# Kernel optimization log

Measured on AMD Instinct MI355X. Metric: run time of the kernel, lower is better.

## Reference

```python
import jax, jax.numpy as jnp
import numpy as np

N_NODES = 25000
N_EDGES = 400000
N_GRAPHS = 1000
HID = 185
IN_CH = 9
EPS = 1e-5  # BatchNorm eps (eval mode: uses running stats)


def setup_inputs() -> dict:
    key = jax.random.key(0)
    ks = jax.random.split(key, 12)
    x = jax.random.normal(ks[0], (N_NODES, IN_CH), jnp.float32)
    edge_index = jax.random.randint(ks[1], (2, N_EDGES), 0, N_NODES, jnp.int32)
    batch = jnp.sort(jax.random.randint(ks[2], (N_NODES,), 0, N_GRAPHS, jnp.int32))
    W0 = jax.random.normal(ks[3], (IN_CH, HID), jnp.float32) * 0.3
    b0 = jnp.zeros((HID,), jnp.float32)
    W_h = jax.random.normal(ks[4], (3, HID, HID), jnp.float32) * 0.07
    b_h = jnp.zeros((3, HID), jnp.float32)
    bn_gamma = 1.0 + 0.1 * jax.random.normal(ks[5], (4, HID), jnp.float32)
    bn_beta = 0.1 * jax.random.normal(ks[6], (4, HID), jnp.float32)
    bn_mean = 0.1 * jax.random.normal(ks[7], (4, HID), jnp.float32)
    bn_var = jax.random.uniform(ks[8], (4, HID), jnp.float32, 0.5, 1.5)
    W_jk = jax.random.normal(ks[9], (4 * HID, HID), jnp.float32) * 0.05
    b_jk = jnp.zeros((HID,), jnp.float32)
    W_out = jax.random.normal(ks[10], (HID, 1), jnp.float32) * 0.1
    b_out = jnp.zeros((1,), jnp.float32)
    return dict(x=x, edge_index=edge_index, batch=batch, W0=W0, b0=b0,
                W_h=W_h, b_h=b_h, bn_gamma=bn_gamma, bn_beta=bn_beta,
                bn_mean=bn_mean, bn_var=bn_var, W_jk=W_jk, b_jk=b_jk,
                W_out=W_out, b_out=b_out)


def reference(x, edge_index, batch, W0, b0, W_h, b_h, bn_gamma, bn_beta,
              bn_mean, bn_var, W_jk, b_jk, W_out, b_out):
    N = x.shape[0]
    # GCN normalization with self-loops (gcn_norm, edge_weight = 1)
    loop = jnp.arange(N, dtype=edge_index.dtype)
    src = jnp.concatenate([edge_index[0], loop])  # [E+N]
    dst = jnp.concatenate([edge_index[1], loop])  # [E+N]
    deg = jax.ops.segment_sum(jnp.ones_like(dst, dtype=x.dtype), dst, num_segments=N)
    dis = jnp.where(deg > 0, jax.lax.rsqrt(jnp.maximum(deg, 1.0)), 0.0)
    enorm = dis[src] * dis[dst]  # [E+N]

    def gcn_conv(h, W, b):
        h = h @ W                                   # [N, HID]
        msg = h[src] * enorm[:, None]               # gather + scale, [E+N, HID]
        return jax.ops.segment_sum(msg, dst, num_segments=N) + b

    def bn_relu(h, i):
        h = (h - bn_mean[i]) * jax.lax.rsqrt(bn_var[i] + EPS) * bn_gamma[i] + bn_beta[i]
        return jax.nn.relu(h)  # dropout is identity in eval mode

    xs = []
    h = bn_relu(gcn_conv(x, W0, b0), 0)
    xs.append(h)
    for i in range(3):
        h = bn_relu(gcn_conv(h, W_h[i], b_h[i]), i + 1)
        xs.append(h)
    # JumpingKnowledge 'cat' + internal lin (740 -> 185)
    h = jnp.concatenate(xs, axis=-1) @ W_jk + b_jk  # [N, HID]
    # global_max_pool over graphs
    pooled = jax.ops.segment_max(h, batch, num_segments=N_GRAPHS)  # [G, HID]
    return pooled @ W_out + b_out  # [G, 1]
```

## Files before the change

### kernel.cpp

```cpp
#include <hip/hip_runtime.h>
#include <hip/hip_bf16.h>

#define N_NODES 25000
#define N_EDGES 400000
#define N_GRAPHS 1000
#define HID 185
#define EPS 1e-5f
#define XPITCH 768
#define APITCH 36

typedef __attribute__((ext_vector_type(8))) short bf16x8;
typedef __attribute__((ext_vector_type(4))) float f32x4;

__device__ __forceinline__ short f2bf(float f) {
    union { float f; unsigned u; } v; v.f = f;
    unsigned r = v.u + 0x7FFFu + ((v.u >> 16) & 1u);
    return (short)(r >> 16);
}
__device__ __forceinline__ float bfl(unsigned u) { return __uint_as_float(u << 16); }
__device__ __forceinline__ float bfh(unsigned u) { return __uint_as_float(u & 0xFFFF0000u); }
__device__ __forceinline__ unsigned pk2(float lo, float hi) {
    return (unsigned)(unsigned short)f2bf(lo) | ((unsigned)(unsigned short)f2bf(hi) << 16);
}

__global__ void k_init(int* cnt, int* cursor) {
    int i = blockIdx.x * blockDim.x + threadIdx.x;
    if (i < N_NODES) { cnt[i] = 0; cursor[i] = 0; }
}

__global__ void k_deg(const int* __restrict__ dst, int* cnt, int E) {
    int i = blockIdx.x * blockDim.x + threadIdx.x;
    if (i < E) atomicAdd(&cnt[dst[i]], 1);
}

__global__ void k_dis(const int* __restrict__ cnt, float* dis, int N) {
    int i = blockIdx.x * blockDim.x + threadIdx.x;
    if (i < N) dis[i] = rsqrtf((float)(cnt[i] + 1));
}

__global__ __launch_bounds__(256) void k_scan_part(const int* __restrict__ cnt,
                                                   int* __restrict__ bsum, int N) {
    int i = blockIdx.x * 256 + threadIdx.x;
    int v = (i < N) ? cnt[i] : 0;
    #pragma unroll
    for (int off = 32; off; off >>= 1) v += __shfl_down(v, off);
    __shared__ int s[4];
    if ((threadIdx.x & 63) == 0) s[threadIdx.x >> 6] = v;
    __syncthreads();
    if (threadIdx.x == 0) bsum[blockIdx.x] = s[0] + s[1] + s[2] + s[3];
}

__global__ __launch_bounds__(128) void k_scan_mid(const int* __restrict__ bsum,
                                                  int* __restrict__ boff, int NB) {
    __shared__ int s[128];
    int t = threadIdx.x;
    int v = (t < NB) ? bsum[t] : 0;
    s[t] = v; __syncthreads();
    for (int off = 1; off < 128; off <<= 1) {
        int x = (t >= off) ? s[t - off] : 0;
        __syncthreads();
        s[t] += x;
        __syncthreads();
    }
    if (t < NB) boff[t] = s[t] - v;
}

__global__ __launch_bounds__(256) void k_scan_add(const int* __restrict__ cnt,
                                                  const int* __restrict__ boff,
                                                  int* __restrict__ rowptr, int N) {
    __shared__ int s[256];
    int t = threadIdx.x;
    int i = blockIdx.x * 256 + t;
    int v = (i < N) ? cnt[i] : 0;
    s[t] = v; __syncthreads();
    for (int off = 1; off < 256; off <<= 1) {
        int x = (t >= off) ? s[t - off] : 0;
        __syncthreads();
        s[t] += x;
        __syncthreads();
    }
    if (i < N) rowptr[i + 1] = boff[blockIdx.x] + s[t];
    if (i == 0) rowptr[0] = 0;
}

__global__ void k_scatter(const int* __restrict__ src, const int* __restrict__ dst,
                          const float* __restrict__ dis, const int* __restrict__ rowptr,
                          int* cursor, int* __restrict__ csr_src,
                          float* __restrict__ csr_w, int E) {
    int e = blockIdx.x * blockDim.x + threadIdx.x;
    if (e < E) {
        int d = dst[e];
        int s = src[e];
        int pos = atomicAdd(&cursor[d], 1);
        int o = rowptr[d] + pos;
        csr_src[o] = s;
        csr_w[o] = dis[s];
    }
}

__global__ void k_prep_w(const float* __restrict__ W_h, const float* __restrict__ W_jk,
                         const float* __restrict__ b0, const float* __restrict__ b_h,
                         const float* __restrict__ gamma, const float* __restrict__ beta,
                         const float* __restrict__ mean, const float* __restrict__ var,
                         short* __restrict__ Wt_h, short* __restrict__ Wt_jk,
                         float* __restrict__ bnsc, float* __restrict__ bnsh) {
    int idx = blockIdx.x * 256 + threadIdx.x;
    const int HW = 3 * 192 * 192;
    const int JW = 192 * 768;
    if (idx < HW) {
        int l = idx / (192 * 192);
        int r = idx % (192 * 192);
        int n = r / 192, k = r % 192;
        float v = (n < HID && k < HID) ? W_h[(l * HID + k) * HID + n] : 0.0f;
        Wt_h[idx] = f2bf(v);
    } else if (idx < HW + JW) {
        int j2 = idx - HW;
        int n = j2 / 768, kk = j2 % 768;
        int l = kk / 192, j = kk % 192;
        float v = (n < HID && j < HID) ? W_jk[(l * HID + j) * HID + n] : 0.0f;
        Wt_jk[j2] = f2bf(v);
    } else if (idx < HW + JW + 4 * 192) {
        int li = idx - HW - JW;
        int l = li / 192, c = li % 192;
        float sc = 0.0f, sh = 0.0f;
        if (c < HID) {
            float bb = (l == 0) ? b0[c] : b_h[(l - 1) * HID + c];
            sc = rsqrtf(var[l * HID + c] + EPS) * gamma[l * HID + c];
            sh = (bb - mean[l * HID + c]) * sc + beta[l * HID + c];
        }
        bnsc[li] = sc;
        bnsh[li] = sh;
    }
}

__global__ void k_aggr0(const float* __restrict__ x, const float* __restrict__ dis,
                        const int* __restrict__ rowptr, const int* __restrict__ csr_src,
                        const float* __restrict__ csr_w, float* __restrict__ xa, int N) {
    int idx = blockIdx.x * blockDim.x + threadIdx.x;
    int n = idx >> 4;
    int c = idx & 15;
    if (n >= N || c >= 9) return;
    float dn = dis[n];
    float acc = x[n * 9 + c] * dn;
    int e = rowptr[n], end = rowptr[n + 1];
    for (; e + 4 <= end; e += 4) {
        int s0 = csr_src[e], s1 = csr_src[e + 1], s2 = csr_src[e + 2], s3 = csr_src[e + 3];
        float w0 = csr_w[e], w1 = csr_w[e + 1], w2 = csr_w[e + 2], w3 = csr_w[e + 3];
        float v0 = x[s0 * 9 + c], v1 = x[s1 * 9 + c], v2 = x[s2 * 9 + c], v3 = x[s3 * 9 + c];
        acc += v0 * w0 + v1 * w1 + v2 * w2 + v3 * w3;
    }
    for (; e < end; ++e)
        acc += x[csr_src[e] * 9 + c] * csr_w[e];
    xa[n * 9 + c] = acc * dn;
}

__global__ __launch_bounds__(192) void k_gemm0(const float* __restrict__ A,
                                               const float* __restrict__ W,
                                               const float* __restrict__ bnsc,
                                               const float* __restrict__ bnsh,
                                               short* __restrict__ xcat, int N) {
    __shared__ float As[8 * 9];
    const int tid = threadIdx.x;
    const int r0 = blockIdx.x * 8;
    for (int idx = tid; idx < 72; idx += 192) {
        int r = idx & 7, k = idx >> 3;
        int row = r0 + r;
        As[idx] = (row < N) ? A[row * 9 + k] : 0.0f;
    }
    __syncthreads();
    const int c = tid;
    float res[8];
    #pragma unroll
    for (int r = 0; r < 8; ++r) res[r] = 0.0f;
    if (c < HID) {
        float acc[8] = {0,0,0,0,0,0,0,0};
        for (int k = 0; k < 9; ++k) {
            float w = W[k * HID + c];
            #pragma unroll
            for (int r = 0; r < 8; ++r) acc[r] += As[k * 8 + r] * w;
        }
        float sc = bnsc[c], sh = bnsh[c];
        #pragma unroll
        for (int r = 0; r < 8; ++r)
            res[r] = fmaxf(acc[r] * sc + sh, 0.0f);
    }
    #pragma unroll
    for (int r = 0; r < 8; ++r) {
        int row = r0 + r;
        if (row < N) xcat[row * XPITCH + c] = (c < HID) ? f2bf(res[r]) : (short)0;
    }
}

template<int KCH, bool F32OUT>
__global__ __launch_bounds__(256) void k_mgemm(const short* __restrict__ A,
                                               const short* __restrict__ Bt,
                                               void* __restrict__ Cout, int N) {
    __shared__ short As[64 * APITCH];
    __shared__ short Bs[192 * APITCH];
    const int tid = threadIdx.x;
    const int wave = tid >> 6;
    const int lane = tid & 63;
    const int quad = lane >> 4;
    const int lm = lane & 15;
    const int r0 = blockIdx.x * 64;
    const int KTOT = KCH * 32;
    const int arow = tid >> 2, aseg = tid & 3;

    f32x4 acc[4][3];
    #pragma unroll
    for (int i = 0; i < 4; ++i)
        #pragma unroll
        for (int j = 0; j < 3; ++j) acc[i][j] = (f32x4){0.f, 0.f, 0.f, 0.f};

    for (int kc = 0; kc < KCH; ++kc) {
        const int k0 = kc * 32;
        {
            int grow = r0 + arow;
            bf16x8 v = (bf16x8){0,0,0,0,0,0,0,0};
            if (grow < N) v = *(const bf16x8*)(A + grow * XPITCH + k0 + aseg * 8);
            *(bf16x8*)(As + arow * APITCH + aseg * 8) = v;
        }
        #pragma unroll
        for (int i = 0; i < 3; ++i) {
            int u = tid + i * 256;
            int n = u >> 2, seg = u & 3;
            bf16x8 v = *(const bf16x8*)(Bt + n * KTOT + k0 + seg * 8);
            *(bf16x8*)(Bs + n * APITCH + seg * 8) = v;
        }
        __syncthreads();
        bf16x8 a[4], b[3];
        #pragma unroll
        for (int mt = 0; mt < 4; ++mt)
            a[mt] = *(const bf16x8*)(As + (mt * 16 + lm) * APITCH + quad * 8);
        #pragma unroll
        for (int nt = 0; nt < 3; ++nt)
            b[nt] = *(const bf16x8*)(Bs + (wave * 48 + nt * 16 + lm) * APITCH + quad * 8);
        #pragma unroll
        for (int mt = 0; mt < 4; ++mt)
            #pragma unroll
            for (int nt = 0; nt < 3; ++nt)
                acc[mt][nt] = __builtin_amdgcn_mfma_f32_16x16x32_bf16(a[mt], b[nt], acc[mt][nt], 0, 0, 0);
        __syncthreads();
    }
    #pragma unroll
    for (int mt = 0; mt < 4; ++mt) {
        #pragma unroll
        for (int nt = 0; nt < 3; ++nt) {
            int col = wave * 48 + nt * 16 + lm;
            #pragma unroll
            for (int r = 0; r < 4; ++r) {
                int row = r0 + mt * 16 + quad * 4 + r;
                if (row < N) {
                    if (F32OUT) ((float*)Cout)[row * 192 + col] = acc[mt][nt][r];
                    else        ((short*)Cout)[row * 192 + col] = f2bf(acc[mt][nt][r]);
                }
            }
        }
    }
}

__global__ __launch_bounds__(256) void k_aggr_bn(const short* __restrict__ tmp16,
                                                 const float* __restrict__ dis,
                                                 const int* __restrict__ rowptr,
                                                 const int* __restrict__ csr_src,
                                                 const float* __restrict__ csr_w,
                                                 const float* __restrict__ bnsc,
                                                 const float* __restrict__ bnsh,
                                                 short* __restrict__ outp, int N) {
    int n = (blockIdx.x << 2) + (threadIdx.x >> 6);
    if (n >= N) return;
    int lane = threadIdx.x & 63;
    int c0 = (lane < 48) ? (lane << 2) : 0;
    float dn = dis[n];
    float a0, a1, a2, a3;
    {
        uint2 v = *(const uint2*)(tmp16 + (size_t)n * 192 + c0);
        a0 = bfl(v.x) * dn; a1 = bfh(v.x) * dn; a2 = bfl(v.y) * dn; a3 = bfh(v.y) * dn;
    }
    int e = rowptr[n], end = rowptr[n + 1];
    for (; e + 4 <= end; e += 4) {
        int s0 = csr_src[e], s1 = csr_src[e + 1], s2 = csr_src[e + 2], s3 = csr_src[e + 3];
        float w0 = csr_w[e], w1 = csr_w[e + 1], w2 = csr_w[e + 2], w3 = csr_w[e + 3];
        uint2 v0 = *(const uint2*)(tmp16 + (size_t)s0 * 192 + c0);
        uint2 v1 = *(const uint2*)(tmp16 + (size_t)s1 * 192 + c0);
        uint2 v2 = *(const uint2*)(tmp16 + (size_t)s2 * 192 + c0);
        uint2 v3 = *(const uint2*)(tmp16 + (size_t)s3 * 192 + c0);
        a0 += bfl(v0.x) * w0; a1 += bfh(v0.x) * w0; a2 += bfl(v0.y) * w0; a3 += bfh(v0.y) * w0;
        a0 += bfl(v1.x) * w1; a1 += bfh(v1.x) * w1; a2 += bfl(v1.y) * w1; a3 += bfh(v1.y) * w1;
        a0 += bfl(v2.x) * w2; a1 += bfh(v2.x) * w2; a2 += bfl(v2.y) * w2; a3 += bfh(v2.y) * w2;
        a0 += bfl(v3.x) * w3; a1 += bfh(v3.x) * w3; a2 += bfl(v3.y) * w3; a3 += bfh(v3.y) * w3;
    }
    for (; e < end; ++e) {
        int s = csr_src[e];
        float w = csr_w[e];
        uint2 v = *(const uint2*)(tmp16 + (size_t)s * 192 + c0);
        a0 += bfl(v.x) * w; a1 += bfh(v.x) * w; a2 += bfl(v.y) * w; a3 += bfh(v.y) * w;
    }
    float4 sc = *(const float4*)(bnsc + c0);
    float4 sh = *(const float4*)(bnsh + c0);
    float o0 = fmaxf(a0 * dn * sc.x + sh.x, 0.0f);
    float o1 = fmaxf(a1 * dn * sc.y + sh.y, 0.0f);
    float o2 = fmaxf(a2 * dn * sc.z + sh.z, 0.0f);
    float o3 = fmaxf(a3 * dn * sc.w + sh.w, 0.0f);
    if (lane < 48) {
        uint2 p;
        p.x = pk2(o0, o1);
        p.y = pk2(o2, o3);
        *(uint2*)(outp + (size_t)n * XPITCH + c0) = p;
    }
}

__global__ __launch_bounds__(192) void k_pool_out(const float* __restrict__ tmpf,
                                                  const int* __restrict__ batch,
                                                  const float* __restrict__ b_jk,
                                                  const float* __restrict__ W_out,
                                                  const float* __restrict__ b_out,
                                                  float* __restrict__ out, int N) {
    __shared__ int bounds[2];
    __shared__ float partial[3];
    const int g = blockIdx.x;
    const int tid = threadIdx.x;
    if (tid < 2) {
        int key = g + tid;
        int lo = 0, hi = N;
        while (lo < hi) {
            int mid = (lo + hi) >> 1;
            if (batch[mid] < key) lo = mid + 1; else hi = mid;
        }
        bounds[tid] = lo;
    }
    __syncthreads();
    const int beg = bounds[0], end = bounds[1];
    float mx = -3.4e38f;
    for (int n = beg; n < end; ++n)
        mx = fmaxf(mx, tmpf[(size_t)n * 192 + tid]);
    float p = (tid < HID) ? (mx + b_jk[tid]) * W_out[tid] : 0.0f;
    #pragma unroll
    for (int off = 32; off; off >>= 1) p += __shfl_down(p, off);
    if ((tid & 63) == 0) partial[tid >> 6] = p;
    __syncthreads();
    if (tid == 0) out[g] = partial[0] + partial[1] + partial[2] + b_out[0];
}

extern "C" void kernel_launch(void* const* d_in, const int* in_sizes, int n_in,
                              void* d_out, int out_size, void* d_ws, size_t ws_size,
                              hipStream_t stream) {
    const float* x      = (const float*)d_in[0];
    const int*   ei     = (const int*)  d_in[1];
    const int*   batch  = (const int*)  d_in[2];
    const float* W0     = (const float*)d_in[3];
    const float* b0     = (const float*)d_in[4];
    const float* W_h    = (const float*)d_in[5];
    const float* b_h    = (const float*)d_in[6];
    const float* gamma  = (const float*)d_in[7];
    const float* beta   = (const float*)d_in[8];
    const float* mean   = (const float*)d_in[9];
    const float* var    = (const float*)d_in[10];
    const float* W_jk   = (const float*)d_in[11];
    const float* b_jk   = (const float*)d_in[12];
    const float* W_out  = (const float*)d_in[13];
    const float* b_out  = (const float*)d_in[14];
    float* out = (float*)d_out;

    const int N = N_NODES, E = N_EDGES, G = N_GRAPHS, H = HID;
    const int NB = (N + 255) / 256;

    float* dis   = (float*)d_ws;
    float* xa    = dis + 25024;
    float* csr_w = xa + 225024;
    float* bnsc  = csr_w + 400000;
    float* bnsh  = bnsc + 768;
    float* tmpf  = bnsh + 768;
    short* xcat  = (short*)(tmpf + 4800000);
    short* tmp16 = xcat + 19200000;
    short* Wt_h  = tmp16 + 4800000;
    short* Wt_jk = Wt_h + 110592;
    int* rowptr  = (int*)(Wt_jk + 147456);
    int* cnt     = rowptr + 25024;
    int* cursor  = cnt + 25024;
    int* csr_src = cursor + 25024;
    int* bsum    = csr_src + 400000;
    int* boff    = bsum + 128;

    const int* src = ei;
    const int* dst = ei + E;

    k_init<<<NB, 256, 0, stream>>>(cnt, cursor);
    k_deg<<<(E + 255) / 256, 256, 0, stream>>>(dst, cnt, E);
    k_dis<<<NB, 256, 0, stream>>>(cnt, dis, N);
    k_scan_part<<<NB, 256, 0, stream>>>(cnt, bsum, N);
    k_scan_mid<<<1, 128, 0, stream>>>(bsum, boff, NB);
    k_scan_add<<<NB, 256, 0, stream>>>(cnt, boff, rowptr, N);
    k_scatter<<<(E + 255) / 256, 256, 0, stream>>>(src, dst, dis, rowptr, cursor,
                                                   csr_src, csr_w, E);
    k_prep_w<<<(3 * 192 * 192 + 192 * 768 + 4 * 192 + 255) / 256, 256, 0, stream>>>(
        W_h, W_jk, b0, b_h, gamma, beta, mean, var, Wt_h, Wt_jk, bnsc, bnsh);

    k_aggr0<<<(N * 16 + 255) / 256, 256, 0, stream>>>(x, dis, rowptr, csr_src, csr_w, xa, N);
    k_gemm0<<<(N + 7) / 8, 192, 0, stream>>>(xa, W0, bnsc, bnsh, xcat, N);

    const int MB = (N + 63) / 64;
    for (int l = 1; l < 4; ++l) {
        k_mgemm<6, false><<<MB, 256, 0, stream>>>(xcat + (l - 1) * 192,
                                                  Wt_h + (l - 1) * 192 * 192, tmp16, N);
        k_aggr_bn<<<(N + 3) / 4, 256, 0, stream>>>(tmp16, dis, rowptr, csr_src, csr_w,
                                                   bnsc + l * 192, bnsh + l * 192,
                                                   xcat + l * 192, N);
    }

    k_mgemm<24, true><<<MB, 256, 0, stream>>>(xcat, Wt_jk, tmpf, N);

    k_pool_out<<<G, 192, 0, stream>>>(tmpf, batch, b_jk, W_out, b_out, out, N);
}
```

Baseline: 315.8 us.

## Double-buffer A tiles via direct global-to-LDS loads, keep B in registers, bf16 JK output

The MFMA GEMM now streams A tiles into a double-buffered, XOR-swizzled LDS buffer using global_load_lds. B (weight) fragments are loaded straight into registers for groups of six k-chunks instead of being staged in LDS, which removes the B LDS traffic and one barrier per chunk and lets the next A load overlap compute. The JK GEMM output is stored as bf16 instead of fp32, roughly halving the bytes pooling has to read, at some cost in precision before the max-pool. The separate dis kernel is folded into the scan kernel to save a launch.

```diff
diff --git a/kernel.cpp b/kernel.cpp
--- a/kernel.cpp
+++ b/kernel.cpp
@@ -7,7 +7,6 @@
 #define HID 185
 #define EPS 1e-5f
 #define XPITCH 768
-#define APITCH 36
 
 typedef __attribute__((ext_vector_type(8))) short bf16x8;
 typedef __attribute__((ext_vector_type(4))) float f32x4;
@@ -23,6 +22,10 @@
     return (unsigned)(unsigned short)f2bf(lo) | ((unsigned)(unsigned short)f2bf(hi) << 16);
 }
 
+#define GLD16(g, l) __builtin_amdgcn_global_load_lds( \
+    (const __attribute__((address_space(1))) unsigned*)(const void*)(g), \
+    (__attribute__((address_space(3))) unsigned*)(void*)(l), 16, 0, 0)
+
 __global__ void k_init(int* cnt, int* cursor) {
     int i = blockIdx.x * blockDim.x + threadIdx.x;
     if (i < N_NODES) { cnt[i] = 0; cursor[i] = 0; }
@@ -33,15 +36,12 @@
     if (i < E) atomicAdd(&cnt[dst[i]], 1);
 }
 
-__global__ void k_dis(const int* __restrict__ cnt, float* dis, int N) {
-    int i = blockIdx.x * blockDim.x + threadIdx.x;
-    if (i < N) dis[i] = rsqrtf((float)(cnt[i] + 1));
-}
-
 __global__ __launch_bounds__(256) void k_scan_part(const int* __restrict__ cnt,
-                                                   int* __restrict__ bsum, int N) {
+                                                   int* __restrict__ bsum,
+                                                   float* __restrict__ dis, int N) {
     int i = blockIdx.x * 256 + threadIdx.x;
     int v = (i < N) ? cnt[i] : 0;
+    if (i < N) dis[i] = rsqrtf((float)(v + 1));
     #pragma unroll
     for (int off = 32; off; off >>= 1) v += __shfl_down(v, off);
     __shared__ int s[4];
@@ -191,12 +191,11 @@
     }
 }
 
-template<int KCH, bool F32OUT>
-__global__ __launch_bounds__(256) void k_mgemm(const short* __restrict__ A,
-                                               const short* __restrict__ Bt,
-                                               void* __restrict__ Cout, int N) {
-    __shared__ short As[64 * APITCH];
-    __shared__ short Bs[192 * APITCH];
+template<int KCH>
+__global__ __launch_bounds__(256, 3) void k_mgemm(const short* __restrict__ A,
+                                                  const short* __restrict__ Bt,
+                                                  short* __restrict__ Cout, int N) {
+    __shared__ short As[2][64 * 32];
     const int tid = threadIdx.x;
     const int wave = tid >> 6;
     const int lane = tid & 63;
@@ -204,7 +203,10 @@
     const int lm = lane & 15;
     const int r0 = blockIdx.x * 64;
     const int KTOT = KCH * 32;
-    const int arow = tid >> 2, aseg = tid & 3;
+    const int srow = tid >> 2;
+    const int sseg = (tid & 3) ^ ((srow >> 1) & 3);
+    const long gbase = (long)(r0 + srow) * XPITCH + sseg * 8;
+    const int axor = (lm >> 1) & 3;
 
     f32x4 acc[4][3];
     #pragma unroll
@@ -212,35 +214,34 @@
         #pragma unroll
         for (int j = 0; j < 3; ++j) acc[i][j] = (f32x4){0.f, 0.f, 0.f, 0.f};
 
-    for (int kc = 0; kc < KCH; ++kc) {
-        const int k0 = kc * 32;
-        {
-            int grow = r0 + arow;
-            bf16x8 v = (bf16x8){0,0,0,0,0,0,0,0};
-            if (grow < N) v = *(const bf16x8*)(A + grow * XPITCH + k0 + aseg * 8);
-            *(bf16x8*)(As + arow * APITCH + aseg * 8) = v;
-        }
+    GLD16(A + gbase, &As[0][tid * 8]);
+
+    #pragma unroll
+    for (int g = 0; g < KCH / 6; ++g) {
+        bf16x8 b[3][6];
         #pragma unroll
-        for (int i = 0; i < 3; ++i) {
-            int u = tid + i * 256;
-            int n = u >> 2, seg = u & 3;
-            bf16x8 v = *(const bf16x8*)(Bt + n * KTOT + k0 + seg * 8);
-            *(bf16x8*)(Bs + n * APITCH + seg * 8) = v;
-        }
-        __syncthreads();
-        bf16x8 a[4], b[3];
-        #pragma unroll
-        for (int mt = 0; mt < 4; ++mt)
-            a[mt] = *(const bf16x8*)(As + (mt * 16 + lm) * APITCH + quad * 8);
-        #pragma unroll
-        for (int nt = 0; nt < 3; ++nt)
-            b[nt] = *(const bf16x8*)(Bs + (wave * 48 + nt * 16 + lm) * APITCH + quad * 8);
-        #pragma unroll
-        for (int mt = 0; mt < 4; ++mt)
+        for (int j = 0; j < 6; ++j)
             #pragma unroll
             for (int nt = 0; nt < 3; ++nt)
-                acc[mt][nt] = __builtin_amdgcn_mfma_f32_16x16x32_bf16(a[mt], b[nt], acc[mt][nt], 0, 0, 0);
-        __syncthreads();
+                b[nt][j] = *(const bf16x8*)(Bt + (wave * 48 + nt * 16 + lm) * KTOT
+                                            + (g * 6 + j) * 32 + quad * 8);
+        #pragma unroll
+        for (int j = 0; j < 6; ++j) {
+            const int kc = g * 6 + j;
+            __syncthreads();
+            if (kc + 1 < KCH)
+                GLD16(A + gbase + (kc + 1) * 32, &As[(kc + 1) & 1][tid * 8]);
+            bf16x8 a[4];
+            #pragma unroll
+            for (int mt = 0; mt < 4; ++mt)
+                a[mt] = *(const bf16x8*)(&As[kc & 1][(mt * 16 + lm) * 32 + (quad ^ axor) * 8]);
+            #pragma unroll
+            for (int mt = 0; mt < 4; ++mt)
+                #pragma unroll
+                for (int nt = 0; nt < 3; ++nt)
+                    acc[mt][nt] = __builtin_amdgcn_mfma_f32_16x16x32_bf16(
+                        a[mt], b[nt][j], acc[mt][nt], 0, 0, 0);
+        }
     }
     #pragma unroll
     for (int mt = 0; mt < 4; ++mt) {
@@ -250,10 +251,7 @@
             #pragma unroll
             for (int r = 0; r < 4; ++r) {
                 int row = r0 + mt * 16 + quad * 4 + r;
-                if (row < N) {
-                    if (F32OUT) ((float*)Cout)[row * 192 + col] = acc[mt][nt][r];
-                    else        ((short*)Cout)[row * 192 + col] = f2bf(acc[mt][nt][r]);
-                }
+                if (row < N) Cout[row * 192 + col] = f2bf(acc[mt][nt][r]);
             }
         }
     }
@@ -310,7 +308,7 @@
     }
 }
 
-__global__ __launch_bounds__(192) void k_pool_out(const float* __restrict__ tmpf,
+__global__ __launch_bounds__(192) void k_pool_out(const short* __restrict__ jk,
                                                   const int* __restrict__ batch,
                                                   const float* __restrict__ b_jk,
                                                   const float* __restrict__ W_out,
@@ -333,7 +331,7 @@
     const int beg = bounds[0], end = bounds[1];
     float mx = -3.4e38f;
     for (int n = beg; n < end; ++n)
-        mx = fmaxf(mx, tmpf[(size_t)n * 192 + tid]);
+        mx = fmaxf(mx, bfl((unsigned)(unsigned short)jk[(size_t)n * 192 + tid]));
     float p = (tid < HID) ? (mx + b_jk[tid]) * W_out[tid] : 0.0f;
     #pragma unroll
     for (int off = 32; off; off >>= 1) p += __shfl_down(p, off);
@@ -370,8 +368,7 @@
     float* csr_w = xa + 225024;
     float* bnsc  = csr_w + 400000;
     float* bnsh  = bnsc + 768;
-    float* tmpf  = bnsh + 768;
-    short* xcat  = (short*)(tmpf + 4800000);
+    short* xcat  = (short*)(bnsh + 768);
     short* tmp16 = xcat + 19200000;
     short* Wt_h  = tmp16 + 4800000;
     short* Wt_jk = Wt_h + 110592;
@@ -387,8 +384,7 @@
 
     k_init<<<NB, 256, 0, stream>>>(cnt, cursor);
     k_deg<<<(E + 255) / 256, 256, 0, stream>>>(dst, cnt, E);
-    k_dis<<<NB, 256, 0, stream>>>(cnt, dis, N);
-    k_scan_part<<<NB, 256, 0, stream>>>(cnt, bsum, N);
+    k_scan_part<<<NB, 256, 0, stream>>>(cnt, bsum, dis, N);
     k_scan_mid<<<1, 128, 0, stream>>>(bsum, boff, NB);
     k_scan_add<<<NB, 256, 0, stream>>>(cnt, boff, rowptr, N);
     k_scatter<<<(E + 255) / 256, 256, 0, stream>>>(src, dst, dis, rowptr, cursor,
@@ -401,14 +397,14 @@
 
     const int MB = (N + 63) / 64;
     for (int l = 1; l < 4; ++l) {
-        k_mgemm<6, false><<<MB, 256, 0, stream>>>(xcat + (l - 1) * 192,
-                                                  Wt_h + (l - 1) * 192 * 192, tmp16, N);
+        k_mgemm<6><<<MB, 256, 0, stream>>>(xcat + (l - 1) * 192,
+                                           Wt_h + (l - 1) * 192 * 192, tmp16, N);
         k_aggr_bn<<<(N + 3) / 4, 256, 0, stream>>>(tmp16, dis, rowptr, csr_src, csr_w,
                                                    bnsc + l * 192, bnsh + l * 192,
                                                    xcat + l * 192, N);
     }
 
-    k_mgemm<24, true><<<MB, 256, 0, stream>>>(xcat, Wt_jk, tmpf, N);
-
-    k_pool_out<<<G, 192, 0, stream>>>(tmpf, batch, b_jk, W_out, b_out, out, N);
-}
+    k_mgemm<24><<<MB, 256, 0, stream>>>(xcat, Wt_jk, tmp16, N);
+
+    k_pool_out<<<G, 192, 0, stream>>>(tmp16, batch, b_jk, W_out, b_out, out, N);
+}
```

Measured after the change: 317.3 us. About the same (+0.5%).
